# Performance work log

Hardware: AMD Instinct MI355X
Metric: run time of the kernel (lower is better)

Reference implementation:

```python
import jax, jax.numpy as jnp
import numpy as np

TOPK = 0.1  # fraction of h*w spatial positions, from __init__ default


def setup_inputs() -> dict:
    key = jax.random.key(0)
    x = jax.random.normal(key, (32, 256, 56, 56), dtype=jnp.float32)
    return {"x": x}


def reference(x) -> jnp.ndarray:
    # Faithful translation of TopKLayer.sparse_hw (including its quirky
    # comparison of ascending *ranks* against the spatial *index* of the
    # k-th largest element, exactly as the torch code does).
    n, c, h, w = x.shape
    k = int(max(1, TOPK * h * w))  # topk_keep_num = 313 for 56x56
    x_r = x.reshape(n * c, h * w)              # (nc, hw)
    abs_x = jnp.abs(x_r)
    # ranks[i, j] = ascending rank of abs_x[i, j] within row i
    ranks = jnp.argsort(jnp.argsort(abs_x, axis=1), axis=1)
    # spatial index of the k-th largest |x| in each row
    thr_idx = jax.lax.top_k(abs_x, k)[1][:, -1]  # (nc,)
    mask = (ranks < thr_idx[:, None]).reshape(n, c, h, w)
    return x * mask.astype(x.dtype)
```

## Files before the change

### kernel.cpp

```cpp
#include <hip/hip_runtime.h>
#include <stdint.h>


#define HW   3136
#define NT   256
#define KSEL 313u
#define NB0  2048
#define SP0  (NB0 / NT)
#define CAP  512

__device__ __forceinline__ unsigned block_scan_incl(unsigned v, unsigned* wt) {
    const int lane = threadIdx.x & 63;
    const int w = threadIdx.x >> 6;
    for (int d = 1; d < 64; d <<= 1) {
        unsigned o = __shfl_up(v, d, 64);
        if (lane >= d) v += o;
    }
    if (lane == 63) wt[w] = v;
    __syncthreads();
    unsigned add = 0;
    for (int i = 0; i < w; ++i) add += wt[i];
    __syncthreads();
    return v + add;
}

template <bool fromTop>
__device__ void locate0(const unsigned* hist, unsigned rank,
                        unsigned* wt, unsigned* s_b) {
    const int t = threadIdx.x;
    const int base = t * SP0;
    unsigned g = 0;
#pragma unroll
    for (int i = 0; i < SP0; ++i) {
        int b = fromTop ? (NB0 - 1 - (base + i)) : (base + i);
        g += hist[b];
    }
    unsigned S = block_scan_incl(g, wt);
    if (S >= rank && (S - g) < rank) {
        unsigned lr = rank - (S - g);
        unsigned acc = 0;
        for (int i = 0; i < SP0; ++i) {
            int b = fromTop ? (NB0 - 1 - (base + i)) : (base + i);
            unsigned h = hist[b];
            acc += h;
            if (acc >= lr) { s_b[0] = (unsigned)b; s_b[1] = lr - (acc - h); break; }
        }
    }
    if (t == 0) s_b[3] = 0;
    __syncthreads();
}

template <bool fromTop>
__device__ void select_stable(const uint4* s_x4, const unsigned* hist0,
                              unsigned* cand, unsigned* wt, unsigned* s_b,
                              unsigned rank, unsigned& keyOut, unsigned& eOut) {
    const int t = threadIdx.x;
    locate0<fromTop>(hist0, rank, wt, s_b);
    const unsigned b0 = s_b[0];
    const unsigned m  = s_b[1];

    for (int j = t; j < HW / 4; j += NT) {
        uint4 v = s_x4[j];
        const unsigned i0 = 4u * (unsigned)j;
        unsigned k;
        k = v.x & 0x7fffffffu;
        if ((k >> 20) == b0) { unsigned p = atomicAdd(&s_b[3], 1u); if (p < CAP) cand[p] = ((k & 0xFFFFFu) << 12) | i0; }
        k = v.y & 0x7fffffffu;
        if ((k >> 20) == b0) { unsigned p = atomicAdd(&s_b[3], 1u); if (p < CAP) cand[p] = ((k & 0xFFFFFu) << 12) | (i0 + 1u); }
        k = v.z & 0x7fffffffu;
        if ((k >> 20) == b0) { unsigned p = atomicAdd(&s_b[3], 1u); if (p < CAP) cand[p] = ((k & 0xFFFFFu) << 12) | (i0 + 2u); }
        k = v.w & 0x7fffffffu;
        if ((k >> 20) == b0) { unsigned p = atomicAdd(&s_b[3], 1u); if (p < CAP) cand[p] = ((k & 0xFFFFFu) << 12) | (i0 + 3u); }
    }
    __syncthreads();
    const unsigned cnt = s_b[3];

    if (cnt <= CAP) {
        for (int i = t; i < (int)cnt; i += NT) {
            const unsigned ci = cand[i];
            const unsigned Ci = fromTop ? (ci ^ 0xFFFu) : ci;
            unsigned r = 1;
            for (int j = 0; j < (int)cnt; ++j) {
                const unsigned Cj = fromTop ? (cand[j] ^ 0xFFFu) : cand[j];
                if (fromTop ? (Cj > Ci) : (Cj < Ci)) r++;
            }
            if (r == m) s_b[2] = ci;
        }
        __syncthreads();
        const unsigned ci = s_b[2];
        keyOut = (b0 << 20) | (ci >> 12);
        eOut = ci & 0xFFFu;
    } else {
        const unsigned* s_x = (const unsigned*)s_x4;
        for (int j = t; j < HW; j += NT) {
            const unsigned k = s_x[j] & 0x7fffffffu;
            if ((k >> 20) != b0) continue;
            unsigned Ci = ((k & 0xFFFFFu) << 12) | (unsigned)j;
            if (fromTop) Ci ^= 0xFFFu;
            unsigned r = 1;
            for (int j2 = 0; j2 < HW; ++j2) {
                const unsigned k2 = s_x[j2] & 0x7fffffffu;
                if ((k2 >> 20) != b0) continue;
                unsigned Cj = ((k2 & 0xFFFFFu) << 12) | (unsigned)j2;
                if (fromTop) Cj ^= 0xFFFu;
                if (fromTop ? (Cj > Ci) : (Cj < Ci)) r++;
            }
            if (r == m) s_b[2] = ((k & 0xFFFFFu) << 12) | (unsigned)j;
        }
        __syncthreads();
        const unsigned ci = s_b[2];
        keyOut = (b0 << 20) | (ci >> 12);
        eOut = ci & 0xFFFu;
    }
}

extern "C" __global__ void __launch_bounds__(NT)
topk_kernel(const float* __restrict__ x, float* __restrict__ out) {
    __shared__ uint4 s_x4[HW / 4];
    __shared__ unsigned s_hist0[NB0];
    __shared__ unsigned s_cand[CAP];
    __shared__ unsigned s_wt[4];
    __shared__ unsigned s_b[4];

    const int t = threadIdx.x;
    const int row = blockIdx.x;
    const uint4* __restrict__ xin = (const uint4*)(x + (size_t)row * HW);
    uint4* __restrict__ xout = (uint4*)(out + (size_t)row * HW);

    for (int i = t; i < NB0; i += NT) s_hist0[i] = 0;
    __syncthreads();
    for (int j = t; j < HW / 4; j += NT) {
        uint4 v = xin[j];
        s_x4[j] = v;
        atomicAdd(&s_hist0[(v.x & 0x7fffffffu) >> 20], 1u);
        atomicAdd(&s_hist0[(v.y & 0x7fffffffu) >> 20], 1u);
        atomicAdd(&s_hist0[(v.z & 0x7fffffffu) >> 20], 1u);
        atomicAdd(&s_hist0[(v.w & 0x7fffffffu) >> 20], 1u);
    }
    __syncthreads();

    unsigned KA, tIdx;
    select_stable<true>(s_x4, s_hist0, s_cand, s_wt, s_b, KSEL, KA, tIdx);

    if (tIdx == 0) {
        uint4 z = make_uint4(0u, 0u, 0u, 0u);
        for (int j = t; j < HW / 4; j += NT) xout[j] = z;
        return;
    }

    unsigned KB, eB;
    select_stable<false>(s_x4, s_hist0, s_cand, s_wt, s_b, tIdx, KB, eB);

    for (int j = t; j < HW / 4; j += NT) {
        uint4 v = s_x4[j];
        const unsigned i0 = 4u * (unsigned)j;
        unsigned k;
        k = v.x & 0x7fffffffu; if (!(k < KB || (k == KB && i0      <= eB))) v.x = 0u;
        k = v.y & 0x7fffffffu; if (!(k < KB || (k == KB && i0 + 1u <= eB))) v.y = 0u;
        k = v.z & 0x7fffffffu; if (!(k < KB || (k == KB && i0 + 2u <= eB))) v.z = 0u;
        k = v.w & 0x7fffffffu; if (!(k < KB || (k == KB && i0 + 3u <= eB))) v.w = 0u;
        xout[j] = v;
    }
}

extern "C" void kernel_launch(void* const* d_in, const int* in_sizes, int n_in,
                              void* d_out, int out_size, void* d_ws, size_t ws_size,
                              hipStream_t stream) {
    const float* x = (const float*)d_in[0];
    float* out = (float*)d_out;
    const int rows = in_sizes[0] / HW;
    topk_kernel<<<dim3(rows), dim3(NT), 0, stream>>>(x, out);
}
```

Baseline: 71.59 us.

## Pack histogram into 16-bit padded bins and refine candidates with second-level wave histogram

The 2048-bin histogram is packed as pairs of 16-bit counters in padded 32-bit words, which halves its shared-memory footprint and reduces bank conflicts. Bin location now runs in a single wavefront using a shuffle scan and ballot, with no block-wide scan barriers. Candidates in the selected bin are narrowed further by a second-level 256-bin histogram on their upper bits. Only a small set of at most 64 is then ranked quadratically, replacing the O(cnt^2) ranking over up to 512 candidates. If either candidate buffer overflows, the code falls back to the full quadratic scan.

```diff
diff --git a/kernel.cpp b/kernel.cpp
--- a/kernel.cpp
+++ b/kernel.cpp
@@ -2,156 +2,206 @@
 #include <stdint.h>
 
 
-#define HW   3136
-#define NT   256
-#define KSEL 313u
-#define NB0  2048
-#define SP0  (NB0 / NT)
-#define CAP  512
-
-__device__ __forceinline__ unsigned block_scan_incl(unsigned v, unsigned* wt) {
+#define HW    3136
+#define NW4   784
+#define NT    256
+#define KSEL  313u
+#define CAP   320
+#define CAP2  64
+
+#define PADW(w) ((w) + ((w) >> 4))
+
+__device__ __forceinline__ unsigned wscan(unsigned v) {
     const int lane = threadIdx.x & 63;
-    const int w = threadIdx.x >> 6;
+#pragma unroll
     for (int d = 1; d < 64; d <<= 1) {
         unsigned o = __shfl_up(v, d, 64);
         if (lane >= d) v += o;
     }
-    if (lane == 63) wt[w] = v;
-    __syncthreads();
-    unsigned add = 0;
-    for (int i = 0; i < w; ++i) add += wt[i];
-    __syncthreads();
-    return v + add;
+    return v;
+}
+
+__device__ __forceinline__ unsigned h16(const unsigned* h, unsigned bin) {
+    unsigned w = h[PADW(bin >> 1)];
+    return (bin & 1) ? (w >> 16) : (w & 0xFFFFu);
+}
+
+__device__ __forceinline__ void hadd(unsigned* h, unsigned bin) {
+    atomicAdd(&h[PADW(bin >> 1)], (bin & 1) ? 0x10000u : 1u);
+}
+
+template <int SEGW, bool fromTop>
+__device__ void locate(const unsigned* h, unsigned m, unsigned& bOut, unsigned& mOut) {
+    const int lane = threadIdx.x & 63;
+    const int seg = fromTop ? (63 - lane) : lane;
+    unsigned s = 0;
+#pragma unroll
+    for (int i = 0; i < SEGW; ++i) {
+        unsigned w = h[PADW(seg * SEGW + i)];
+        s += (w & 0xFFFFu) + (w >> 16);
+    }
+    unsigned S = wscan(s);
+    unsigned long long bal = __ballot(S >= m);
+    int fl = __ffsll(bal) - 1;
+    unsigned packed = 0;
+    if (lane == fl) {
+        unsigned rem = m - (S - s);
+        unsigned acc = 0;
+        const int nb = SEGW * 2;
+        for (int i = 0; i < nb; ++i) {
+            unsigned bin = fromTop ? (unsigned)(seg * nb + nb - 1 - i)
+                                   : (unsigned)(seg * nb + i);
+            unsigned hh = h16(h, bin);
+            acc += hh;
+            if (acc >= rem) { packed = (bin << 16) | (rem - (acc - hh)); break; }
+        }
+    }
+    packed = __shfl(packed, fl, 64);
+    bOut = packed >> 16;
+    mOut = packed & 0xFFFFu;
 }
 
 template <bool fromTop>
-__device__ void locate0(const unsigned* hist, unsigned rank,
-                        unsigned* wt, unsigned* s_b) {
+__device__ void rank_cand_wave(unsigned* h2, const unsigned* cand, unsigned* tiny,
+                               unsigned* s_b, unsigned cnt, unsigned m) {
+    const int lane = threadIdx.x & 63;
+    for (int i = lane; i < 136; i += 64) h2[i] = 0;
+    for (int i = lane; i < (int)cnt; i += 64) hadd(h2, cand[i] >> 24);
+    unsigned b2, m2;
+    locate<2, fromTop>(h2, m, b2, m2);
+    if (lane == 0) s_b[5] = 0;
+    for (int i = lane; i < (int)cnt; i += 64) {
+        unsigned c = cand[i];
+        if ((c >> 24) == b2) {
+            unsigned p = atomicAdd(&s_b[5], 1u);
+            if (p < CAP2) tiny[p] = c;
+        }
+    }
+    unsigned c2 = s_b[5];
+    if (c2 > CAP2) { if (lane == 0) s_b[4] = 1u; return; }
+    if (lane < (int)c2) {
+        unsigned ci = tiny[lane];
+        unsigned di = fromTop ? (ci ^ 0xFFFu) : ci;
+        unsigned r = 1;
+        for (unsigned j = 0; j < c2; ++j) {
+            unsigned dj = fromTop ? (tiny[j] ^ 0xFFFu) : tiny[j];
+            if (fromTop ? (dj > di) : (dj < di)) r++;
+        }
+        if (r == m2) s_b[2] = ci;
+    }
+}
+
+template <bool fromTop>
+__device__ void block_select(const uint4* s_x4, const unsigned* s_h0,
+                             unsigned* s_cand, unsigned* s_h2, unsigned* s_tiny,
+                             unsigned* s_b, unsigned rank,
+                             unsigned& keyOut, unsigned& eOut) {
     const int t = threadIdx.x;
-    const int base = t * SP0;
-    unsigned g = 0;
-#pragma unroll
-    for (int i = 0; i < SP0; ++i) {
-        int b = fromTop ? (NB0 - 1 - (base + i)) : (base + i);
-        g += hist[b];
-    }
-    unsigned S = block_scan_incl(g, wt);
-    if (S >= rank && (S - g) < rank) {
-        unsigned lr = rank - (S - g);
-        unsigned acc = 0;
-        for (int i = 0; i < SP0; ++i) {
-            int b = fromTop ? (NB0 - 1 - (base + i)) : (base + i);
-            unsigned h = hist[b];
-            acc += h;
-            if (acc >= lr) { s_b[0] = (unsigned)b; s_b[1] = lr - (acc - h); break; }
-        }
-    }
-    if (t == 0) s_b[3] = 0;
-    __syncthreads();
-}
-
-template <bool fromTop>
-__device__ void select_stable(const uint4* s_x4, const unsigned* hist0,
-                              unsigned* cand, unsigned* wt, unsigned* s_b,
-                              unsigned rank, unsigned& keyOut, unsigned& eOut) {
-    const int t = threadIdx.x;
-    locate0<fromTop>(hist0, rank, wt, s_b);
+    const int lane = t & 63;
+    const int wid = t >> 6;
+
+    if (wid == 0) {
+        unsigned b0, m1;
+        locate<16, fromTop>(s_h0, rank, b0, m1);
+        if (lane == 0) { s_b[0] = b0; s_b[1] = m1; s_b[3] = 0; s_b[4] = 0; }
+    }
+    __syncthreads();
     const unsigned b0 = s_b[0];
-    const unsigned m  = s_b[1];
-
-    for (int j = t; j < HW / 4; j += NT) {
+    const unsigned m1 = s_b[1];
+
+    for (int j = t; j < NW4; j += NT) {
         uint4 v = s_x4[j];
         const unsigned i0 = 4u * (unsigned)j;
-        unsigned k;
+        unsigned k, p;
         k = v.x & 0x7fffffffu;
-        if ((k >> 20) == b0) { unsigned p = atomicAdd(&s_b[3], 1u); if (p < CAP) cand[p] = ((k & 0xFFFFFu) << 12) | i0; }
+        if ((k >> 20) == b0) { p = atomicAdd(&s_b[3], 1u); if (p < CAP) s_cand[p] = ((k & 0xFFFFFu) << 12) | i0; }
         k = v.y & 0x7fffffffu;
-        if ((k >> 20) == b0) { unsigned p = atomicAdd(&s_b[3], 1u); if (p < CAP) cand[p] = ((k & 0xFFFFFu) << 12) | (i0 + 1u); }
+        if ((k >> 20) == b0) { p = atomicAdd(&s_b[3], 1u); if (p < CAP) s_cand[p] = ((k & 0xFFFFFu) << 12) | (i0 + 1u); }
         k = v.z & 0x7fffffffu;
-        if ((k >> 20) == b0) { unsigned p = atomicAdd(&s_b[3], 1u); if (p < CAP) cand[p] = ((k & 0xFFFFFu) << 12) | (i0 + 2u); }
+        if ((k >> 20) == b0) { p = atomicAdd(&s_b[3], 1u); if (p < CAP) s_cand[p] = ((k & 0xFFFFFu) << 12) | (i0 + 2u); }
         k = v.w & 0x7fffffffu;
-        if ((k >> 20) == b0) { unsigned p = atomicAdd(&s_b[3], 1u); if (p < CAP) cand[p] = ((k & 0xFFFFFu) << 12) | (i0 + 3u); }
+        if ((k >> 20) == b0) { p = atomicAdd(&s_b[3], 1u); if (p < CAP) s_cand[p] = ((k & 0xFFFFFu) << 12) | (i0 + 3u); }
     }
     __syncthreads();
     const unsigned cnt = s_b[3];
 
+    bool needFallback;
     if (cnt <= CAP) {
-        for (int i = t; i < (int)cnt; i += NT) {
-            const unsigned ci = cand[i];
-            const unsigned Ci = fromTop ? (ci ^ 0xFFFu) : ci;
-            unsigned r = 1;
-            for (int j = 0; j < (int)cnt; ++j) {
-                const unsigned Cj = fromTop ? (cand[j] ^ 0xFFFu) : cand[j];
-                if (fromTop ? (Cj > Ci) : (Cj < Ci)) r++;
-            }
-            if (r == m) s_b[2] = ci;
-        }
+        if (wid == 0) rank_cand_wave<fromTop>(s_h2, s_cand, s_tiny, s_b, cnt, m1);
         __syncthreads();
-        const unsigned ci = s_b[2];
-        keyOut = (b0 << 20) | (ci >> 12);
-        eOut = ci & 0xFFFu;
+        needFallback = (s_b[4] != 0);
     } else {
-        const unsigned* s_x = (const unsigned*)s_x4;
-        for (int j = t; j < HW; j += NT) {
-            const unsigned k = s_x[j] & 0x7fffffffu;
-            if ((k >> 20) != b0) continue;
-            unsigned Ci = ((k & 0xFFFFFu) << 12) | (unsigned)j;
-            if (fromTop) Ci ^= 0xFFFu;
-            unsigned r = 1;
-            for (int j2 = 0; j2 < HW; ++j2) {
-                const unsigned k2 = s_x[j2] & 0x7fffffffu;
-                if ((k2 >> 20) != b0) continue;
-                unsigned Cj = ((k2 & 0xFFFFFu) << 12) | (unsigned)j2;
-                if (fromTop) Cj ^= 0xFFFu;
-                if (fromTop ? (Cj > Ci) : (Cj < Ci)) r++;
-            }
-            if (r == m) s_b[2] = ((k & 0xFFFFFu) << 12) | (unsigned)j;
-        }
-        __syncthreads();
-        const unsigned ci = s_b[2];
-        keyOut = (b0 << 20) | (ci >> 12);
-        eOut = ci & 0xFFFu;
-    }
+        needFallback = true;
+    }
+
+    if (!needFallback) {
+        const unsigned c = s_b[2];
+        keyOut = (b0 << 20) | (c >> 12);
+        eOut = c & 0xFFFu;
+        return;
+    }
+
+    const unsigned* s_x = (const unsigned*)s_x4;
+    for (int j = t; j < HW; j += NT) {
+        const unsigned k = s_x[j] & 0x7fffffffu;
+        if ((k >> 20) != b0) continue;
+        unsigned Ci = ((k & 0xFFFFFu) << 12) | (unsigned)j;
+        if (fromTop) Ci ^= 0xFFFu;
+        unsigned r = 1;
+        for (int j2 = 0; j2 < HW; ++j2) {
+            const unsigned k2 = s_x[j2] & 0x7fffffffu;
+            if ((k2 >> 20) != b0) continue;
+            unsigned Cj = ((k2 & 0xFFFFFu) << 12) | (unsigned)j2;
+            if (fromTop) Cj ^= 0xFFFu;
+            if (fromTop ? (Cj > Ci) : (Cj < Ci)) r++;
+        }
+        if (r == m1) s_b[2] = ((k & 0xFFFFFu) << 12) | (unsigned)j;
+    }
+    __syncthreads();
+    const unsigned c = s_b[2];
+    keyOut = (b0 << 20) | (c >> 12);
+    eOut = c & 0xFFFu;
 }
 
 extern "C" __global__ void __launch_bounds__(NT)
 topk_kernel(const float* __restrict__ x, float* __restrict__ out) {
-    __shared__ uint4 s_x4[HW / 4];
-    __shared__ unsigned s_hist0[NB0];
+    __shared__ uint4 s_x4[NW4];
+    __shared__ unsigned s_h0[1088];
     __shared__ unsigned s_cand[CAP];
-    __shared__ unsigned s_wt[4];
-    __shared__ unsigned s_b[4];
+    __shared__ unsigned s_h2[136];
+    __shared__ unsigned s_tiny[CAP2];
+    __shared__ unsigned s_b[8];
 
     const int t = threadIdx.x;
     const int row = blockIdx.x;
     const uint4* __restrict__ xin = (const uint4*)(x + (size_t)row * HW);
     uint4* __restrict__ xout = (uint4*)(out + (size_t)row * HW);
 
-    for (int i = t; i < NB0; i += NT) s_hist0[i] = 0;
-    __syncthreads();
-    for (int j = t; j < HW / 4; j += NT) {
+    for (int i = t; i < 1088; i += NT) s_h0[i] = 0;
+    __syncthreads();
+    for (int j = t; j < NW4; j += NT) {
         uint4 v = xin[j];
         s_x4[j] = v;
-        atomicAdd(&s_hist0[(v.x & 0x7fffffffu) >> 20], 1u);
-        atomicAdd(&s_hist0[(v.y & 0x7fffffffu) >> 20], 1u);
-        atomicAdd(&s_hist0[(v.z & 0x7fffffffu) >> 20], 1u);
-        atomicAdd(&s_hist0[(v.w & 0x7fffffffu) >> 20], 1u);
+        hadd(s_h0, (v.x & 0x7fffffffu) >> 20);
+        hadd(s_h0, (v.y & 0x7fffffffu) >> 20);
+        hadd(s_h0, (v.z & 0x7fffffffu) >> 20);
+        hadd(s_h0, (v.w & 0x7fffffffu) >> 20);
     }
     __syncthreads();
 
     unsigned KA, tIdx;
-    select_stable<true>(s_x4, s_hist0, s_cand, s_wt, s_b, KSEL, KA, tIdx);
+    block_select<true>(s_x4, s_h0, s_cand, s_h2, s_tiny, s_b, KSEL, KA, tIdx);
 
     if (tIdx == 0) {
         uint4 z = make_uint4(0u, 0u, 0u, 0u);
-        for (int j = t; j < HW / 4; j += NT) xout[j] = z;
+        for (int j = t; j < NW4; j += NT) xout[j] = z;
         return;
     }
 
     unsigned KB, eB;
-    select_stable<false>(s_x4, s_hist0, s_cand, s_wt, s_b, tIdx, KB, eB);
-
-    for (int j = t; j < HW / 4; j += NT) {
+    block_select<false>(s_x4, s_h0, s_cand, s_h2, s_tiny, s_b, tIdx, KB, eB);
+
+    for (int j = t; j < NW4; j += NT) {
         uint4 v = s_x4[j];
         const unsigned i0 = 4u * (unsigned)j;
         unsigned k;
```

Result: slower. 82.09 us (+14.7%).

## Process one row per wavefront with register-resident data and packed LDS histogram

Applied to the files above, without the earlier changes.

Each 64-lane wavefront now owns a whole row, so the block-wide scans and __syncthreads disappear in favour of wave shuffles and ballots. The row is kept in registers instead of shared memory. The 2048-bin histogram is packed as 16-bit pairs to cut LDS use and raise occupancy, and a second-level 256-bin histogram narrows the candidates before an O(n^2) rank over at most 64 items. The cost is heavy register pressure from 12 uint4 values per lane, and a fallback path that rereads global memory when candidate caps overflow.

```diff
diff --git a/kernel.cpp b/kernel.cpp
--- a/kernel.cpp
+++ b/kernel.cpp
@@ -2,164 +2,238 @@
 #include <stdint.h>
 
 
-#define HW   3136
-#define NT   256
-#define KSEL 313u
-#define NB0  2048
-#define SP0  (NB0 / NT)
-#define CAP  512
-
-__device__ __forceinline__ unsigned block_scan_incl(unsigned v, unsigned* wt) {
+#define HW     3136
+#define NT     128
+#define WPB    2
+#define KSEL   313u
+#define CAP    448
+#define CAP2   64
+#define SLICE  1088
+#define O_CAND 0
+#define O_HC   448
+#define O_TINY 704
+#define M31    0x7fffffffu
+
+__device__ __forceinline__ unsigned wscan_incl(unsigned v) {
     const int lane = threadIdx.x & 63;
-    const int w = threadIdx.x >> 6;
+#pragma unroll
     for (int d = 1; d < 64; d <<= 1) {
         unsigned o = __shfl_up(v, d, 64);
         if (lane >= d) v += o;
     }
-    if (lane == 63) wt[w] = v;
-    __syncthreads();
-    unsigned add = 0;
-    for (int i = 0; i < w; ++i) add += wt[i];
-    __syncthreads();
-    return v + add;
+    return v;
+}
+
+__device__ __forceinline__ unsigned bcast_first(unsigned flag, unsigned val) {
+    unsigned long long bal = __ballot(flag != 0);
+    int fl = __ffsll(bal) - 1;
+    return __shfl(val, fl, 64);
+}
+
+__device__ __forceinline__ void hadd(unsigned* h, unsigned b) {
+    atomicAdd(&h[(b >> 1) + (b >> 5)], (b & 1) ? 0x10000u : 1u);
 }
 
 template <bool fromTop>
-__device__ void locate0(const unsigned* hist, unsigned rank,
-                        unsigned* wt, unsigned* s_b) {
-    const int t = threadIdx.x;
-    const int base = t * SP0;
-    unsigned g = 0;
-#pragma unroll
-    for (int i = 0; i < SP0; ++i) {
-        int b = fromTop ? (NB0 - 1 - (base + i)) : (base + i);
-        g += hist[b];
-    }
-    unsigned S = block_scan_incl(g, wt);
-    if (S >= rank && (S - g) < rank) {
-        unsigned lr = rank - (S - g);
-        unsigned acc = 0;
-        for (int i = 0; i < SP0; ++i) {
-            int b = fromTop ? (NB0 - 1 - (base + i)) : (base + i);
-            unsigned h = hist[b];
-            acc += h;
-            if (acc >= lr) { s_b[0] = (unsigned)b; s_b[1] = lr - (acc - h); break; }
-        }
-    }
-    if (t == 0) s_b[3] = 0;
-    __syncthreads();
-}
-
-template <bool fromTop>
-__device__ void select_stable(const uint4* s_x4, const unsigned* hist0,
-                              unsigned* cand, unsigned* wt, unsigned* s_b,
-                              unsigned rank, unsigned& keyOut, unsigned& eOut) {
-    const int t = threadIdx.x;
-    locate0<fromTop>(hist0, rank, wt, s_b);
-    const unsigned b0 = s_b[0];
-    const unsigned m  = s_b[1];
-
-    for (int j = t; j < HW / 4; j += NT) {
-        uint4 v = s_x4[j];
-        const unsigned i0 = 4u * (unsigned)j;
-        unsigned k;
-        k = v.x & 0x7fffffffu;
-        if ((k >> 20) == b0) { unsigned p = atomicAdd(&s_b[3], 1u); if (p < CAP) cand[p] = ((k & 0xFFFFFu) << 12) | i0; }
-        k = v.y & 0x7fffffffu;
-        if ((k >> 20) == b0) { unsigned p = atomicAdd(&s_b[3], 1u); if (p < CAP) cand[p] = ((k & 0xFFFFFu) << 12) | (i0 + 1u); }
-        k = v.z & 0x7fffffffu;
-        if ((k >> 20) == b0) { unsigned p = atomicAdd(&s_b[3], 1u); if (p < CAP) cand[p] = ((k & 0xFFFFFu) << 12) | (i0 + 2u); }
-        k = v.w & 0x7fffffffu;
-        if ((k >> 20) == b0) { unsigned p = atomicAdd(&s_b[3], 1u); if (p < CAP) cand[p] = ((k & 0xFFFFFu) << 12) | (i0 + 3u); }
-    }
-    __syncthreads();
-    const unsigned cnt = s_b[3];
-
-    if (cnt <= CAP) {
-        for (int i = t; i < (int)cnt; i += NT) {
-            const unsigned ci = cand[i];
-            const unsigned Ci = fromTop ? (ci ^ 0xFFFu) : ci;
-            unsigned r = 1;
-            for (int j = 0; j < (int)cnt; ++j) {
-                const unsigned Cj = fromTop ? (cand[j] ^ 0xFFFu) : cand[j];
-                if (fromTop ? (Cj > Ci) : (Cj < Ci)) r++;
-            }
-            if (r == m) s_b[2] = ci;
-        }
-        __syncthreads();
-        const unsigned ci = s_b[2];
-        keyOut = (b0 << 20) | (ci >> 12);
-        eOut = ci & 0xFFFu;
-    } else {
-        const unsigned* s_x = (const unsigned*)s_x4;
-        for (int j = t; j < HW; j += NT) {
-            const unsigned k = s_x[j] & 0x7fffffffu;
+__device__ __forceinline__ void wave_select(
+        unsigned* sl, const unsigned* __restrict__ gx,
+        const uint4* v, unsigned vx,
+        const unsigned* pc, unsigned base,
+        unsigned rank, unsigned& keyOut, unsigned& idxOut) {
+    const int lane = threadIdx.x & 63;
+
+    unsigned packed1 = 0;
+    {
+        unsigned run = base;
+#pragma unroll
+        for (int i = 0; i < 32; ++i) {
+            const unsigned cb = (i & 1) ? (pc[i >> 1] >> 16) : (pc[i >> 1] & 0xFFFFu);
+            if (fromTop) {
+                const unsigned suf = HW - run - cb;
+                if (suf < rank && rank <= suf + cb)
+                    packed1 = ((unsigned)(lane * 32 + i) << 16) | (rank - suf);
+            } else {
+                if (run < rank && rank <= run + cb)
+                    packed1 = ((unsigned)(lane * 32 + i) << 16) | (rank - run);
+            }
+            run += cb;
+        }
+    }
+    packed1 = bcast_first(packed1, packed1);
+    const unsigned b0 = packed1 >> 16;
+    const unsigned m1 = packed1 & 0xFFFFu;
+
+    unsigned cc = 0;
+#pragma unroll
+    for (int i = 0; i < 12; ++i) {
+        cc += (((v[i].x & M31) >> 20) == b0);
+        cc += (((v[i].y & M31) >> 20) == b0);
+        cc += (((v[i].z & M31) >> 20) == b0);
+        cc += (((v[i].w & M31) >> 20) == b0);
+    }
+    cc += (((vx & M31) >> 20) == b0);
+    const unsigned cin = wscan_incl(cc);
+    const unsigned cnt = __shfl(cin, 63, 64);
+    bool fb = (cnt > CAP);
+    unsigned result = 0;
+
+    if (!fb) {
+        unsigned pos = cin - cc;
+#pragma unroll
+        for (int i = 0; i < 12; ++i) {
+            const unsigned i0 = 4u * (unsigned)(lane + 64 * i);
+            unsigned k;
+            k = v[i].x & M31; if ((k >> 20) == b0) sl[O_CAND + pos++] = ((k & 0xFFFFFu) << 12) | i0;
+            k = v[i].y & M31; if ((k >> 20) == b0) sl[O_CAND + pos++] = ((k & 0xFFFFFu) << 12) | (i0 + 1u);
+            k = v[i].z & M31; if ((k >> 20) == b0) sl[O_CAND + pos++] = ((k & 0xFFFFFu) << 12) | (i0 + 2u);
+            k = v[i].w & M31; if ((k >> 20) == b0) sl[O_CAND + pos++] = ((k & 0xFFFFFu) << 12) | (i0 + 3u);
+        }
+        { const unsigned k = vx & M31;
+          if ((k >> 20) == b0) sl[O_CAND + pos++] = ((k & 0xFFFFFu) << 12) | (3072u + (unsigned)lane); }
+
+#pragma unroll
+        for (int i = 0; i < 4; ++i) sl[O_HC + lane + 64 * i] = 0;
+        for (unsigned i = lane; i < cnt; i += 64)
+            atomicAdd(&sl[O_HC + (sl[O_CAND + i] >> 24)], 1u);
+
+        unsigned hh[4];
+#pragma unroll
+        for (int i = 0; i < 4; ++i) hh[i] = sl[O_HC + 4 * lane + i];
+        const unsigned s4 = hh[0] + hh[1] + hh[2] + hh[3];
+        unsigned run2 = wscan_incl(s4) - s4;
+        unsigned packed2 = 0;
+#pragma unroll
+        for (int i = 0; i < 4; ++i) {
+            if (fromTop) {
+                const unsigned suf = cnt - run2 - hh[i];
+                if (suf < m1 && m1 <= suf + hh[i])
+                    packed2 = ((unsigned)(4 * lane + i) << 16) | (m1 - suf);
+            } else {
+                if (run2 < m1 && m1 <= run2 + hh[i])
+                    packed2 = ((unsigned)(4 * lane + i) << 16) | (m1 - run2);
+            }
+            run2 += hh[i];
+        }
+        packed2 = bcast_first(packed2, packed2);
+        const unsigned b2 = packed2 >> 16;
+        const unsigned m2 = packed2 & 0xFFFFu;
+
+        unsigned tc = 0;
+        for (unsigned i = lane; i < cnt; i += 64) tc += ((sl[O_CAND + i] >> 24) == b2);
+        const unsigned tincl = wscan_incl(tc);
+        const unsigned c2 = __shfl(tincl, 63, 64);
+        if (c2 > CAP2) fb = true;
+        else {
+            unsigned tpos = tincl - tc;
+            for (unsigned i = lane; i < cnt; i += 64) {
+                const unsigned cw = sl[O_CAND + i];
+                if ((cw >> 24) == b2) sl[O_TINY + tpos++] = cw;
+            }
+            unsigned hitf = 0, resv = 0;
+            if ((unsigned)lane < c2) {
+                const unsigned ci = sl[O_TINY + lane];
+                const unsigned di = fromTop ? (ci ^ 0xFFFu) : ci;
+                unsigned r = 1;
+                for (unsigned j = 0; j < c2; ++j) {
+                    const unsigned dj = fromTop ? (sl[O_TINY + j] ^ 0xFFFu) : sl[O_TINY + j];
+                    if (fromTop ? (dj > di) : (dj < di)) r++;
+                }
+                if (r == m2) { hitf = 1; resv = ci; }
+            }
+            result = bcast_first(hitf, resv);
+        }
+    }
+
+    if (fb) {
+        unsigned hitf = 0, resv = 0;
+        for (unsigned j = lane; j < HW; j += 64) {
+            const unsigned k = gx[j] & M31;
             if ((k >> 20) != b0) continue;
-            unsigned Ci = ((k & 0xFFFFFu) << 12) | (unsigned)j;
+            unsigned Ci = ((k & 0xFFFFFu) << 12) | j;
             if (fromTop) Ci ^= 0xFFFu;
             unsigned r = 1;
-            for (int j2 = 0; j2 < HW; ++j2) {
-                const unsigned k2 = s_x[j2] & 0x7fffffffu;
+            for (unsigned j2 = 0; j2 < HW; ++j2) {
+                const unsigned k2 = gx[j2] & M31;
                 if ((k2 >> 20) != b0) continue;
-                unsigned Cj = ((k2 & 0xFFFFFu) << 12) | (unsigned)j2;
+                unsigned Cj = ((k2 & 0xFFFFFu) << 12) | j2;
                 if (fromTop) Cj ^= 0xFFFu;
                 if (fromTop ? (Cj > Ci) : (Cj < Ci)) r++;
             }
-            if (r == m) s_b[2] = ((k & 0xFFFFFu) << 12) | (unsigned)j;
-        }
-        __syncthreads();
-        const unsigned ci = s_b[2];
-        keyOut = (b0 << 20) | (ci >> 12);
-        eOut = ci & 0xFFFu;
-    }
+            if (r == m1) { hitf = 1; resv = ((k & 0xFFFFFu) << 12) | j; }
+        }
+        result = bcast_first(hitf, resv);
+    }
+
+    keyOut = (b0 << 20) | (result >> 12);
+    idxOut = result & 0xFFFu;
 }
 
 extern "C" __global__ void __launch_bounds__(NT)
 topk_kernel(const float* __restrict__ x, float* __restrict__ out) {
-    __shared__ uint4 s_x4[HW / 4];
-    __shared__ unsigned s_hist0[NB0];
-    __shared__ unsigned s_cand[CAP];
-    __shared__ unsigned s_wt[4];
-    __shared__ unsigned s_b[4];
-
-    const int t = threadIdx.x;
-    const int row = blockIdx.x;
-    const uint4* __restrict__ xin = (const uint4*)(x + (size_t)row * HW);
-    uint4* __restrict__ xout = (uint4*)(out + (size_t)row * HW);
-
-    for (int i = t; i < NB0; i += NT) s_hist0[i] = 0;
-    __syncthreads();
-    for (int j = t; j < HW / 4; j += NT) {
-        uint4 v = xin[j];
-        s_x4[j] = v;
-        atomicAdd(&s_hist0[(v.x & 0x7fffffffu) >> 20], 1u);
-        atomicAdd(&s_hist0[(v.y & 0x7fffffffu) >> 20], 1u);
-        atomicAdd(&s_hist0[(v.z & 0x7fffffffu) >> 20], 1u);
-        atomicAdd(&s_hist0[(v.w & 0x7fffffffu) >> 20], 1u);
-    }
-    __syncthreads();
+    __shared__ unsigned lds[WPB][SLICE];
+    const int lane = threadIdx.x & 63;
+    const int w = threadIdx.x >> 6;
+    const int row = blockIdx.x * WPB + w;
+    unsigned* sl = lds[w];
+    const uint4* __restrict__ xin4 = (const uint4*)(x + (size_t)row * HW);
+    const unsigned* __restrict__ gx = (const unsigned*)xin4;
+    uint4* __restrict__ xout4 = (uint4*)(out + (size_t)row * HW);
+    unsigned* __restrict__ gout = (unsigned*)(out + (size_t)row * HW);
+
+#pragma unroll
+    for (int i = 0; i < 17; ++i) sl[lane + 64 * i] = 0;
+
+    uint4 v[12];
+#pragma unroll
+    for (int i = 0; i < 12; ++i) v[i] = xin4[lane + 64 * i];
+    const unsigned vx = gx[3072 + lane];
+
+#pragma unroll
+    for (int i = 0; i < 12; ++i) {
+        hadd(sl, (v[i].x & M31) >> 20);
+        hadd(sl, (v[i].y & M31) >> 20);
+        hadd(sl, (v[i].z & M31) >> 20);
+        hadd(sl, (v[i].w & M31) >> 20);
+    }
+    hadd(sl, (vx & M31) >> 20);
+
+    unsigned pc[16];
+#pragma unroll
+    for (int i = 0; i < 16; ++i) pc[i] = sl[lane * 17 + i];
+    unsigned ssum = 0;
+#pragma unroll
+    for (int i = 0; i < 16; ++i) ssum += (pc[i] & 0xFFFFu) + (pc[i] >> 16);
+    const unsigned base = wscan_incl(ssum) - ssum;
 
     unsigned KA, tIdx;
-    select_stable<true>(s_x4, s_hist0, s_cand, s_wt, s_b, KSEL, KA, tIdx);
+    wave_select<true>(sl, gx, v, vx, pc, base, KSEL, KA, tIdx);
 
     if (tIdx == 0) {
-        uint4 z = make_uint4(0u, 0u, 0u, 0u);
-        for (int j = t; j < HW / 4; j += NT) xout[j] = z;
+        const uint4 z = make_uint4(0u, 0u, 0u, 0u);
+#pragma unroll
+        for (int i = 0; i < 12; ++i) xout4[lane + 64 * i] = z;
+        gout[3072 + lane] = 0u;
         return;
     }
 
     unsigned KB, eB;
-    select_stable<false>(s_x4, s_hist0, s_cand, s_wt, s_b, tIdx, KB, eB);
-
-    for (int j = t; j < HW / 4; j += NT) {
-        uint4 v = s_x4[j];
-        const unsigned i0 = 4u * (unsigned)j;
+    wave_select<false>(sl, gx, v, vx, pc, base, tIdx, KB, eB);
+
+#pragma unroll
+    for (int i = 0; i < 12; ++i) {
+        const unsigned i0 = 4u * (unsigned)(lane + 64 * i);
+        uint4 o = v[i];
         unsigned k;
-        k = v.x & 0x7fffffffu; if (!(k < KB || (k == KB && i0      <= eB))) v.x = 0u;
-        k = v.y & 0x7fffffffu; if (!(k < KB || (k == KB && i0 + 1u <= eB))) v.y = 0u;
-        k = v.z & 0x7fffffffu; if (!(k < KB || (k == KB && i0 + 2u <= eB))) v.z = 0u;
-        k = v.w & 0x7fffffffu; if (!(k < KB || (k == KB && i0 + 3u <= eB))) v.w = 0u;
-        xout[j] = v;
+        k = o.x & M31; if (!(k < KB || (k == KB && i0      <= eB))) o.x = 0u;
+        k = o.y & M31; if (!(k < KB || (k == KB && i0 + 1u <= eB))) o.y = 0u;
+        k = o.z & M31; if (!(k < KB || (k == KB && i0 + 2u <= eB))) o.z = 0u;
+        k = o.w & M31; if (!(k < KB || (k == KB && i0 + 3u <= eB))) o.w = 0u;
+        xout4[lane + 64 * i] = o;
+    }
+    {
+        const unsigned k = vx & M31;
+        gout[3072 + lane] =
+            (k < KB || (k == KB && (3072u + (unsigned)lane) <= eB)) ? vx : 0u;
     }
 }
 
@@ -169,5 +243,5 @@
     const float* x = (const float*)d_in[0];
     float* out = (float*)d_out;
     const int rows = in_sizes[0] / HW;
-    topk_kernel<<<dim3(rows), dim3(NT), 0, stream>>>(x, out);
-}
+    topk_kernel<<<dim3(rows / WPB), dim3(NT), 0, stream>>>(x, out);
+}
```

Result: faster. 63.48 us (-11.3%).
